# Kernel optimization log

Hardware: AMD Instinct MI355X
Metric: run time of the kernel (lower is better)

## Reference

```python
import jax, jax.numpy as jnp
import numpy as np

N = 100000
E = 1600000
IN_CH = 128
HID = 32
HEADS = 4
OUT_CH = 32
NEG_SLOPE = 0.2


def _gat_layer(x, W, a_src, a_dst, b, src, dst, heads, out_ch):
    """PyG-style GATConv (concat=True). x: [N, F_in]; returns [N, heads*out_ch]."""
    n = x.shape[0]
    h = (x @ W).reshape(n, heads, out_ch)                    # [N, H, C]
    alpha_s = jnp.einsum('nhc,hc->nh', h, a_src)             # [N, H]
    alpha_d = jnp.einsum('nhc,hc->nh', h, a_dst)             # [N, H]
    logits = jax.nn.leaky_relu(alpha_s[src] + alpha_d[dst], NEG_SLOPE)  # [E, H]
    # segment softmax over destination node
    m = jax.ops.segment_max(logits, dst, num_segments=n)
    m = jnp.where(jnp.isfinite(m), m, 0.0)
    p = jnp.exp(logits - m[dst])
    denom = jax.ops.segment_sum(p, dst, num_segments=n)
    alpha = p / (denom[dst] + 1e-16)                         # [E, H]
    msg = h[src] * alpha[..., None]                          # [E, H, C]
    out = jax.ops.segment_sum(msg, dst, num_segments=n)      # [N, H, C]
    return out.reshape(n, heads * out_ch) + b


def setup_inputs() -> dict:
    key = jax.random.key(0)
    ks = jax.random.split(key, 16)
    x = jax.random.normal(ks[0], (N, IN_CH), dtype=jnp.float32)
    edge_index = jax.random.randint(ks[1], (2, E), 0, N, dtype=jnp.int32)

    def glorot(k, shape):
        fan = shape[0] + shape[-1]
        return jax.random.normal(k, shape, dtype=jnp.float32) * np.sqrt(2.0 / fan)

    hid = HID * HEADS  # 128
    return {
        'x': x,
        'edge_index': edge_index,
        'W1': glorot(ks[2], (IN_CH, hid)),
        'a_src1': glorot(ks[3], (HEADS, HID)),
        'a_dst1': glorot(ks[4], (HEADS, HID)),
        'b1': jnp.zeros((hid,), jnp.float32),
        'W2': glorot(ks[5], (hid, hid)),
        'a_src2': glorot(ks[6], (HEADS, HID)),
        'a_dst2': glorot(ks[7], (HEADS, HID)),
        'b2': jnp.zeros((hid,), jnp.float32),
        'W3': glorot(ks[8], (hid, OUT_CH)),
        'a_src3': glorot(ks[9], (1, OUT_CH)),
        'a_dst3': glorot(ks[10], (1, OUT_CH)),
        'b3': jnp.zeros((OUT_CH,), jnp.float32),
    }


def reference(x, edge_index, W1, a_src1, a_dst1, b1, W2, a_src2, a_dst2, b2,
              W3, a_src3, a_dst3, b3):
    # add self-loops (PyG GATConv default add_self_loops=True)
    loop = jnp.arange(N, dtype=edge_index.dtype)
    src = jnp.concatenate([edge_index[0], loop])
    dst = jnp.concatenate([edge_index[1], loop])

    h = _gat_layer(x, W1, a_src1, a_dst1, b1, src, dst, HEADS, HID)
    h = jax.nn.elu(h)
    h = _gat_layer(h, W2, a_src2, a_dst2, b2, src, dst, HEADS, HID)
    h = jax.nn.elu(h)
    out = _gat_layer(h, W3, a_src3, a_dst3, b3, src, dst, 1, OUT_CH)
    return out
```

## Files before the change

### kernel.cpp

```cpp
#include <hip/hip_runtime.h>
#include <cstdint>

#define NN 100000
#define EE 1600000
#define ET (EE + NN)
#define NBUCK 782
#define BCAP 3584

typedef unsigned int u32;
typedef unsigned short u16;
typedef short bf16x8 __attribute__((ext_vector_type(8)));
typedef float f32x4 __attribute__((ext_vector_type(4)));

__device__ __forceinline__ u16 f2bf(float f) {
    union { float f; u32 i; } v; v.f = f;
    u32 r = v.i + 0x7FFFu + ((v.i >> 16) & 1u);
    return (u16)(r >> 16);
}
__device__ __forceinline__ float bf2f(u32 u) {
    union { u32 i; float f; } v; v.i = u << 16; return v.f;
}
__device__ __forceinline__ void get_edge(const int* __restrict__ ei, int e, int& s, int& d) {
    if (e < EE) { s = ei[e]; d = ei[EE + e]; }
    else { s = e - EE; d = s; }
}
__device__ __forceinline__ float leaky(float x) { return x > 0.f ? x : 0.2f * x; }

__global__ __launch_bounds__(256) void wprep_kernel(
    const float* __restrict__ W1, const float* __restrict__ W2, const float* __restrict__ W3,
    u16* __restrict__ wt1, u16* __restrict__ wt2, u16* __restrict__ wt3)
{
    int i = blockIdx.x * 256 + threadIdx.x;
    if (i < 16384)      { int c = i >> 7, k = i & 127; wt1[i] = f2bf(W1[k * 128 + c]); }
    else if (i < 32768) { int j = i - 16384; int c = j >> 7, k = j & 127; wt2[j] = f2bf(W2[k * 128 + c]); }
    else if (i < 36864) { int j = i - 32768; int c = j >> 7, k = j & 127; wt3[j] = f2bf(W3[k * 32 + c]); }
}

template<int OUTC, bool IN16>
__global__ __launch_bounds__(256) void gemm_mfma(
    const void* __restrict__ Xv, const u16* __restrict__ Wt16g,
    const float* __restrict__ asw, const float* __restrict__ adw,
    u16* __restrict__ Hout16, float* __restrict__ as_o, float* __restrict__ ad_o)
{
    constexpr int NT = OUTC / 16;
    constexpr int LDSU = (OUTC == 128) ? 13056 : 6528;
    constexpr int HS = (OUTC == 128) ? 132 : 36;
    __shared__ u32 lds[LDSU];
    u32* wl = lds + 64 * 68;

    const int tid = threadIdx.x;
    const int r0 = blockIdx.x * 64;

    if (IN16) {
        const u32* Xg = (const u32*)Xv;
        for (int i = tid; i < 64 * 64; i += 256) {
            int r = i >> 6, k2 = i & 63;
            u32 v = 0;
            if (r0 + r < NN) v = Xg[(size_t)(r0 + r) * 64 + k2];
            lds[r * 68 + k2] = v;
        }
    } else {
        const float* Xf = (const float*)Xv;
        for (int i = tid; i < 64 * 64; i += 256) {
            int r = i >> 6, k2 = i & 63;
            u32 v = 0;
            if (r0 + r < NN) {
                float2 f = *(const float2*)(Xf + (size_t)(r0 + r) * 128 + k2 * 2);
                v = (u32)f2bf(f.x) | ((u32)f2bf(f.y) << 16);
            }
            lds[r * 68 + k2] = v;
        }
    }
    {
        const u32* Wg = (const u32*)Wt16g;
        for (int i = tid; i < OUTC * 64; i += 256) {
            int c = i >> 6, k2 = i & 63;
            wl[c * 68 + k2] = Wg[i];
        }
    }
    __syncthreads();

    const int w = tid >> 6, l = tid & 63;
    const int lm = l & 15, q = l >> 4;

    f32x4 acc[NT];
    #pragma unroll
    for (int T = 0; T < NT; T++)
        #pragma unroll
        for (int r = 0; r < 4; r++) acc[T][r] = 0.f;

    #pragma unroll
    for (int kc = 0; kc < 4; kc++) {
        bf16x8 af = *(const bf16x8*)&lds[(16 * w + lm) * 68 + kc * 16 + q * 4];
        #pragma unroll
        for (int T = 0; T < NT; T++) {
            bf16x8 bfr = *(const bf16x8*)&wl[(16 * T + lm) * 68 + kc * 16 + q * 4];
            acc[T] = __builtin_amdgcn_mfma_f32_16x16x32_bf16(af, bfr, acc[T], 0, 0, 0);
        }
    }
    __syncthreads();

    float* hl = (float*)lds;
    #pragma unroll
    for (int T = 0; T < NT; T++)
        #pragma unroll
        for (int rg = 0; rg < 4; rg++)
            hl[(16 * w + q * 4 + rg) * HS + 16 * T + lm] = acc[T][rg];
    __syncthreads();

    for (int i = tid; i < 64 * (OUTC / 2); i += 256) {
        int r = i / (OUTC / 2), k2 = i % (OUTC / 2);
        int row = r0 + r;
        if (row < NN) {
            float a = hl[r * HS + k2 * 2];
            float b = hl[r * HS + k2 * 2 + 1];
            ((u32*)Hout16)[(size_t)row * (OUTC / 2) + k2] = (u32)f2bf(a) | ((u32)f2bf(b) << 16);
        }
    }
    if (OUTC == 128) {
        const int row = tid >> 2, part = tid & 3;
        const float* hp = &hl[row * HS + part * 32];
        const float* aw = asw + part * 32;
        const float* dw = adw + part * 32;
        float s = 0.f, d = 0.f;
        #pragma unroll
        for (int c = 0; c < 32; c++) { float hv = hp[c]; s += hv * aw[c]; d += hv * dw[c]; }
        const int grow = r0 + row;
        if (grow < NN) { as_o[(size_t)grow * 4 + part] = s; ad_o[(size_t)grow * 4 + part] = d; }
    } else {
        if (tid < 64) {
            const float* hp = &hl[tid * HS];
            float s = 0.f, d = 0.f;
            #pragma unroll
            for (int c = 0; c < 32; c++) { float hv = hp[c]; s += hv * asw[c]; d += hv * adw[c]; }
            const int grow = r0 + tid;
            if (grow < NN) { as_o[grow] = s; ad_o[grow] = d; }
        }
    }
}

__global__ __launch_bounds__(256) void bin_fill_kernel(const int* __restrict__ ei,
    int* __restrict__ gcur, u32* __restrict__ pairs)
{
    __shared__ int hist[NBUCK];
    __shared__ int base[NBUCK];
    const int t = threadIdx.x;
    for (int i = t; i < NBUCK; i += 256) hist[i] = 0;
    __syncthreads();
    const int chunk = (ET + gridDim.x - 1) / gridDim.x;
    const int e0 = blockIdx.x * chunk;
    const int e1 = min(e0 + chunk, ET);
    for (int e = e0 + t; e < e1; e += 256) {
        int s, d; get_edge(ei, e, s, d);
        atomicAdd(&hist[d >> 7], 1);
    }
    __syncthreads();
    for (int i = t; i < NBUCK; i += 256) {
        int c = hist[i];
        base[i] = c ? atomicAdd(&gcur[i], c) : 0;
        hist[i] = 0;
    }
    __syncthreads();
    for (int e = e0 + t; e < e1; e += 256) {
        int s, d; get_edge(ei, e, s, d);
        int b = d >> 7;
        int pos = atomicAdd(&hist[b], 1);
        pairs[(size_t)b * BCAP + base[b] + pos] = ((u32)(d & 127) << 25) | (u32)s;
    }
}

__global__ __launch_bounds__(1024) void bscan_kernel(const int* __restrict__ bcnt,
    int* __restrict__ bbase, int* __restrict__ rowp)
{
    __shared__ int lds[1024];
    const int t = threadIdx.x;
    int v = (t < NBUCK) ? bcnt[t] : 0;
    lds[t] = v;
    __syncthreads();
    for (int off = 1; off < 1024; off <<= 1) {
        int x = (t >= off) ? lds[t - off] : 0;
        __syncthreads();
        lds[t] += x;
        __syncthreads();
    }
    if (t < NBUCK) bbase[t] = lds[t] - v;
    if (t == 0) { bbase[NBUCK] = ET; rowp[NN] = ET; }
}

__global__ __launch_bounds__(256) void bucket_csr_kernel(const u32* __restrict__ pairs,
    const int* __restrict__ bcnt, const int* __restrict__ bbase,
    int* __restrict__ rowp, int* __restrict__ col)
{
    __shared__ int hist[128], scn[128];
    __shared__ int col_lds[BCAP];
    const int b = blockIdx.x;
    const int cbase = bbase[b];
    const int cnt = bcnt[b];
    const u32* pk0 = pairs + (size_t)b * BCAP;
    const int t = threadIdx.x;
    if (t < 128) hist[t] = 0;
    __syncthreads();
    for (int i = t; i < cnt; i += 256)
        atomicAdd(&hist[pk0[i] >> 25], 1);
    __syncthreads();
    if (t < 128) scn[t] = hist[t];
    __syncthreads();
    for (int off = 1; off < 128; off <<= 1) {
        int x = (t < 128 && t >= off) ? scn[t - off] : 0;
        __syncthreads();
        if (t < 128) scn[t] += x;
        __syncthreads();
    }
    if (t < 128) {
        int ex = scn[t] - hist[t];
        int node = b * 128 + t;
        if (node < NN) rowp[node] = cbase + ex;
        hist[t] = ex;
    }
    __syncthreads();
    for (int i = t; i < cnt; i += 256) {
        u32 pk = pk0[i];
        int pos = atomicAdd(&hist[pk >> 25], 1);
        if (pos < BCAP) col_lds[pos] = pk & 0x1FFFFFFu;
    }
    __syncthreads();
    for (int i = t; i < cnt; i += 256)
        col[cbase + i] = col_lds[i];
}

template<bool DOELU>
__global__ __launch_bounds__(256) void agg4_kernel(
    const int* __restrict__ rowp, const int* __restrict__ col,
    const float* __restrict__ as_, const float* __restrict__ ad_,
    const u16* __restrict__ Hb16, const float* __restrict__ bias,
    u16* __restrict__ outp16)
{
    const int lane = threadIdx.x & 63;
    const int node = blockIdx.x * 4 + (threadIdx.x >> 6);
    const int sub = lane & 15;
    const int h = lane >> 4;

    const int start = rowp[node];
    const int end   = rowp[node + 1];
    const float adv = ad_[(size_t)node * 4 + h];
    const char* hbase = (const char*)Hb16 + lane * 4;
    const float2 bv = *(const float2*)(bias + lane * 2);

    float m = -1e30f, den = 0.f, a0 = 0.f, a1 = 0.f;
    for (int j0 = start; j0 < end; j0 += 16) {
        const int j = j0 + sub;
        const bool valid = (j < end);
        const int s = valid ? col[j] : 0;
        const float lg = valid ? leaky(as_[(size_t)s * 4 + h] + adv) : -1e30f;
        float cm = lg;
        #pragma unroll
        for (int off = 8; off; off >>= 1) cm = fmaxf(cm, __shfl_xor(cm, off));
        const float mnew = fmaxf(m, cm);
        const float sc = __expf(m - mnew);
        a0 *= sc; a1 *= sc; den *= sc; m = mnew;
        const float p = valid ? __expf(lg - m) : 0.f;
        float ps = p;
        #pragma unroll
        for (int off = 8; off; off >>= 1) ps += __shfl_xor(ps, off);
        den += ps;
        const int soff = s << 8;
        int so[16]; float pi[16];
        #pragma unroll
        for (int i = 0; i < 16; i++) {
            so[i] = __shfl(soff, i);
            pi[i] = __shfl(p, (h << 4) | i);
        }
        #pragma unroll
        for (int i = 0; i < 16; i++) {
            u32 wv = *(const u32*)(hbase + so[i]);
            a0 += pi[i] * bf2f(wv & 0xffffu);
            a1 += pi[i] * bf2f(wv >> 16);
        }
    }
    const float rden = 1.f / (den + 1e-16f);
    float v0 = a0 * rden + bv.x;
    float v1 = a1 * rden + bv.y;
    if (DOELU) {
        v0 = v0 > 0.f ? v0 : (__expf(v0) - 1.f);
        v1 = v1 > 0.f ? v1 : (__expf(v1) - 1.f);
    }
    u32 pack = (u32)f2bf(v0) | ((u32)f2bf(v1) << 16);
    *(u32*)(outp16 + (size_t)node * 128 + lane * 2) = pack;
}

__global__ __launch_bounds__(256) void agg1_kernel(
    const int* __restrict__ rowp, const int* __restrict__ col,
    const float* __restrict__ as_, const float* __restrict__ ad_,
    const u16* __restrict__ Hb16, const float* __restrict__ bias,
    float* __restrict__ outp)
{
    const int t = threadIdx.x;
    const int lane = t & 31;
    const int node = blockIdx.x * 8 + (t >> 5);

    const int start = rowp[node];
    const int end   = rowp[node + 1];
    const float adv = ad_[node];
    const char* hbase = (const char*)Hb16 + lane * 2;
    const float bvv = bias[lane];

    float m = -1e30f, den = 0.f, acc = 0.f;
    for (int j0 = start; j0 < end; j0 += 32) {
        const int j = j0 + lane;
        const bool valid = (j < end);
        const int s = valid ? col[j] : 0;
        const float lg = valid ? leaky(as_[s] + adv) : -1e30f;
        float cm = lg;
        #pragma unroll
        for (int off = 16; off; off >>= 1) cm = fmaxf(cm, __shfl_xor(cm, off, 32));
        const float mnew = fmaxf(m, cm);
        const float sc = __expf(m - mnew);
        acc *= sc; den *= sc; m = mnew;
        const float p = valid ? __expf(lg - m) : 0.f;
        float ps = p;
        #pragma unroll
        for (int off = 16; off; off >>= 1) ps += __shfl_xor(ps, off, 32);
        den += ps;
        const int soff = s << 6;
        int so[32]; float pi[32];
        #pragma unroll
        for (int i = 0; i < 32; i++) {
            so[i] = __shfl(soff, i, 32);
            pi[i] = __shfl(p, i, 32);
        }
        #pragma unroll
        for (int i = 0; i < 32; i++)
            acc += pi[i] * bf2f((u32)*(const u16*)(hbase + so[i]));
    }
    outp[(size_t)node * 32 + lane] = acc / (den + 1e-16f) + bvv;
}

extern "C" void kernel_launch(void* const* d_in, const int* in_sizes, int n_in,
                              void* d_out, int out_size, void* d_ws, size_t ws_size,
                              hipStream_t stream)
{
    const float* x   = (const float*)d_in[0];
    const int*   ei  = (const int*)d_in[1];
    const float* W1  = (const float*)d_in[2];
    const float* as1 = (const float*)d_in[3];
    const float* ad1 = (const float*)d_in[4];
    const float* b1  = (const float*)d_in[5];
    const float* W2  = (const float*)d_in[6];
    const float* as2 = (const float*)d_in[7];
    const float* ad2 = (const float*)d_in[8];
    const float* b2  = (const float*)d_in[9];
    const float* W3  = (const float*)d_in[10];
    const float* as3 = (const float*)d_in[11];
    const float* ad3 = (const float*)d_in[12];
    const float* b3  = (const float*)d_in[13];
    float* outp = (float*)d_out;

    char* ws = (char*)d_ws;
    u16*   hb16  = (u16*)(ws);
    u16*   xb16  = (u16*)(ws + 25700000);
    u16*   h3b16 = (u16*)(ws + 51400000);
    float* asb   = (float*)(ws + 57900000);
    float* adb   = (float*)(ws + 59500000);
    int*   rowp  = (int*)(ws + 61100000);
    int*   col   = (int*)(ws + 61600000);
    u32*   pairs = (u32*)(ws + 68400032);
    int*   gcur  = (int*)(ws + 79700000);
    int*   bbase = (int*)(ws + 79704096);
    u16*   wt1   = (u16*)(ws + 79710000);
    u16*   wt2   = (u16*)(ws + 79750000);
    u16*   wt3   = (u16*)(ws + 79790000);

    const dim3 B(256);
    const int gG = (NN + 63) / 64;

    wprep_kernel<<<144, B, 0, stream>>>(W1, W2, W3, wt1, wt2, wt3);
    hipMemsetAsync(gcur, 0, NBUCK * 4, stream);
    bin_fill_kernel<<<256, B, 0, stream>>>(ei, gcur, pairs);
    bscan_kernel<<<1, dim3(1024), 0, stream>>>(gcur, bbase, rowp);
    bucket_csr_kernel<<<NBUCK, B, 0, stream>>>(pairs, gcur, bbase, rowp, col);

    gemm_mfma<128, false><<<gG, B, 0, stream>>>(x, wt1, as1, ad1, hb16, asb, adb);
    agg4_kernel<true><<<NN / 4, B, 0, stream>>>(rowp, col, asb, adb, hb16, b1, xb16);

    gemm_mfma<128, true><<<gG, B, 0, stream>>>(xb16, wt2, as2, ad2, hb16, asb, adb);
    agg4_kernel<true><<<NN / 4, B, 0, stream>>>(rowp, col, asb, adb, hb16, b2, xb16);

    gemm_mfma<32, true><<<gG, B, 0, stream>>>(xb16, wt3, as3, ad3, h3b16, asb, adb);
    agg1_kernel<<<NN / 8, B, 0, stream>>>(rowp, col, asb, adb, h3b16, b3, outp);
}
```

Measured before the change: 461.1 us.

## Fuse layer-1 GEMM, edge binning and weight prep; restructure aggregation per node-group

Merges the weight-prep, edge bin-fill and first-layer GEMM into one heterogeneous kernel launch, with the GEMM converting W1 from fp32 inline. This removes two launches and lets the independent GEMM and binning work run concurrently. The 4-head aggregation is rewritten so a 16-lane group handles a whole node with 16-byte gathers per edge and 8 channels per lane, passing probabilities through LDS instead of shuffles. The aim is more bytes per gather load and fewer shuffle instructions, at the cost of redundant per-head softmax math in every lane and extra LDS traffic.

```diff
diff --git a/kernel.cpp b/kernel.cpp
--- a/kernel.cpp
+++ b/kernel.cpp
@@ -6,6 +6,9 @@
 #define ET (EE + NN)
 #define NBUCK 782
 #define BCAP 3584
+#define G_GEMM 1563
+#define G_FILL 256
+#define G_WPREP 80
 
 typedef unsigned int u32;
 typedef unsigned short u16;
@@ -17,8 +20,11 @@
     u32 r = v.i + 0x7FFFu + ((v.i >> 16) & 1u);
     return (u16)(r >> 16);
 }
-__device__ __forceinline__ float bf2f(u32 u) {
+__device__ __forceinline__ float bf_lo(u32 u) {
     union { u32 i; float f; } v; v.i = u << 16; return v.f;
+}
+__device__ __forceinline__ float bf_hi(u32 u) {
+    union { u32 i; float f; } v; v.i = u & 0xffff0000u; return v.f;
 }
 __device__ __forceinline__ void get_edge(const int* __restrict__ ei, int e, int& s, int& d) {
     if (e < EE) { s = ei[e]; d = ei[EE + e]; }
@@ -26,30 +32,15 @@
 }
 __device__ __forceinline__ float leaky(float x) { return x > 0.f ? x : 0.2f * x; }
 
-__global__ __launch_bounds__(256) void wprep_kernel(
-    const float* __restrict__ W1, const float* __restrict__ W2, const float* __restrict__ W3,
-    u16* __restrict__ wt1, u16* __restrict__ wt2, u16* __restrict__ wt3)
-{
-    int i = blockIdx.x * 256 + threadIdx.x;
-    if (i < 16384)      { int c = i >> 7, k = i & 127; wt1[i] = f2bf(W1[k * 128 + c]); }
-    else if (i < 32768) { int j = i - 16384; int c = j >> 7, k = j & 127; wt2[j] = f2bf(W2[k * 128 + c]); }
-    else if (i < 36864) { int j = i - 32768; int c = j >> 7, k = j & 127; wt3[j] = f2bf(W3[k * 32 + c]); }
-}
-
-template<int OUTC, bool IN16>
-__global__ __launch_bounds__(256) void gemm_mfma(
-    const void* __restrict__ Xv, const u16* __restrict__ Wt16g,
+template<int OUTC, bool IN16, bool WCVT>
+__device__ __forceinline__ void gemm_body(int r0, u32* lds,
+    const void* __restrict__ Xv, const void* __restrict__ Wsrc,
     const float* __restrict__ asw, const float* __restrict__ adw,
-    u16* __restrict__ Hout16, float* __restrict__ as_o, float* __restrict__ ad_o)
+    u16* __restrict__ Hout16, float* __restrict__ as_o, float* __restrict__ ad_o, int tid)
 {
     constexpr int NT = OUTC / 16;
-    constexpr int LDSU = (OUTC == 128) ? 13056 : 6528;
     constexpr int HS = (OUTC == 128) ? 132 : 36;
-    __shared__ u32 lds[LDSU];
     u32* wl = lds + 64 * 68;
-
-    const int tid = threadIdx.x;
-    const int r0 = blockIdx.x * 64;
 
     if (IN16) {
         const u32* Xg = (const u32*)Xv;
@@ -71,8 +62,16 @@
             lds[r * 68 + k2] = v;
         }
     }
-    {
-        const u32* Wg = (const u32*)Wt16g;
+    if (WCVT) {
+        const float* Wf = (const float*)Wsrc;
+        for (int i = tid; i < 128 * 64; i += 256) {
+            int c = i & 127, k2 = i >> 7;
+            float f0 = Wf[(2 * k2) * 128 + c];
+            float f1 = Wf[(2 * k2 + 1) * 128 + c];
+            wl[c * 68 + k2] = (u32)f2bf(f0) | ((u32)f2bf(f1) << 16);
+        }
+    } else {
+        const u32* Wg = (const u32*)Wsrc;
         for (int i = tid; i < OUTC * 64; i += 256) {
             int c = i >> 6, k2 = i & 63;
             wl[c * 68 + k2] = Wg[i];
@@ -139,16 +138,13 @@
     }
 }
 
-__global__ __launch_bounds__(256) void bin_fill_kernel(const int* __restrict__ ei,
-    int* __restrict__ gcur, u32* __restrict__ pairs)
-{
-    __shared__ int hist[NBUCK];
-    __shared__ int base[NBUCK];
-    const int t = threadIdx.x;
+__device__ __forceinline__ void bin_fill_body(int bid, int* hist, int* base,
+    const int* __restrict__ ei, int* __restrict__ gcur, u32* __restrict__ pairs, int t)
+{
     for (int i = t; i < NBUCK; i += 256) hist[i] = 0;
     __syncthreads();
-    const int chunk = (ET + gridDim.x - 1) / gridDim.x;
-    const int e0 = blockIdx.x * chunk;
+    const int chunk = (ET + G_FILL - 1) / G_FILL;
+    const int e0 = bid * chunk;
     const int e1 = min(e0 + chunk, ET);
     for (int e = e0 + t; e < e1; e += 256) {
         int s, d; get_edge(ei, e, s, d);
@@ -167,6 +163,41 @@
         int pos = atomicAdd(&hist[b], 1);
         pairs[(size_t)b * BCAP + base[b] + pos] = ((u32)(d & 127) << 25) | (u32)s;
     }
+}
+
+__global__ __launch_bounds__(256) void fused1_kernel(
+    const float* __restrict__ X, const float* __restrict__ W1,
+    const float* __restrict__ as1, const float* __restrict__ ad1,
+    u16* __restrict__ hb16, float* __restrict__ asb, float* __restrict__ adb,
+    const int* __restrict__ ei, int* __restrict__ gcur, u32* __restrict__ pairs,
+    const float* __restrict__ W2, const float* __restrict__ W3,
+    u16* __restrict__ wt2, u16* __restrict__ wt3)
+{
+    __shared__ __align__(16) u32 smem[13056];
+    const int bid = blockIdx.x;
+    const int tid = threadIdx.x;
+    if (bid < G_GEMM) {
+        gemm_body<128, false, true>(bid * 64, smem, X, W1, as1, ad1, hb16, asb, adb, tid);
+    } else if (bid < G_GEMM + G_FILL) {
+        int* hist = (int*)smem;
+        bin_fill_body(bid - G_GEMM, hist, hist + NBUCK, ei, gcur, pairs, tid);
+    } else {
+        int i = (bid - G_GEMM - G_FILL) * 256 + tid;
+        if (i < 16384)      { int c = i >> 7, k = i & 127; wt2[i] = f2bf(W2[k * 128 + c]); }
+        else                { int j = i - 16384; int c = j >> 7, k = j & 127; wt3[j] = f2bf(W3[k * 32 + c]); }
+    }
+}
+
+template<int OUTC>
+__global__ __launch_bounds__(256) void gemm_mfma(
+    const void* __restrict__ Xv, const u16* __restrict__ Wt16g,
+    const float* __restrict__ asw, const float* __restrict__ adw,
+    u16* __restrict__ Hout16, float* __restrict__ as_o, float* __restrict__ ad_o)
+{
+    constexpr int LDSU = (OUTC == 128) ? 13056 : 6528;
+    __shared__ __align__(16) u32 lds[LDSU];
+    gemm_body<OUTC, true, false>(blockIdx.x * 64, lds, Xv, Wt16g, asw, adw,
+                                 Hout16, as_o, ad_o, threadIdx.x);
 }
 
 __global__ __launch_bounds__(1024) void bscan_kernel(const int* __restrict__ bcnt,
@@ -229,63 +260,109 @@
 }
 
 template<bool DOELU>
-__global__ __launch_bounds__(256) void agg4_kernel(
+__global__ __launch_bounds__(256) void agg4g_kernel(
     const int* __restrict__ rowp, const int* __restrict__ col,
     const float* __restrict__ as_, const float* __restrict__ ad_,
     const u16* __restrict__ Hb16, const float* __restrict__ bias,
     u16* __restrict__ outp16)
 {
-    const int lane = threadIdx.x & 63;
-    const int node = blockIdx.x * 4 + (threadIdx.x >> 6);
+    __shared__ float pex[4 * 288];
+    __shared__ u32   sex[4 * 64];
+    const int tid = threadIdx.x;
+    const int wv = tid >> 6;
+    const int lane = tid & 63;
+    const int g = lane >> 4;
     const int sub = lane & 15;
-    const int h = lane >> 4;
+    const int H = sub >> 2;
+    const int node = blockIdx.x * 16 + wv * 4 + g;
 
     const int start = rowp[node];
     const int end   = rowp[node + 1];
-    const float adv = ad_[(size_t)node * 4 + h];
-    const char* hbase = (const char*)Hb16 + lane * 4;
-    const float2 bv = *(const float2*)(bias + lane * 2);
-
-    float m = -1e30f, den = 0.f, a0 = 0.f, a1 = 0.f;
+    const float4 ad4 = ((const float4*)ad_)[node];
+    const float4* as4 = (const float4*)as_;
+    float* pb = &pex[wv * 288 + g * 68];
+    u32*   sb = &sex[wv * 64 + g * 16];
+    const char* hbase = (const char*)Hb16 + sub * 16;
+
+    float m0 = -1e30f, m1 = -1e30f, m2 = -1e30f, m3 = -1e30f;
+    float d0 = 0.f, d1 = 0.f, d2 = 0.f, d3 = 0.f;
+    float a[8];
+    #pragma unroll
+    for (int i = 0; i < 8; i++) a[i] = 0.f;
+
     for (int j0 = start; j0 < end; j0 += 16) {
         const int j = j0 + sub;
         const bool valid = (j < end);
         const int s = valid ? col[j] : 0;
-        const float lg = valid ? leaky(as_[(size_t)s * 4 + h] + adv) : -1e30f;
-        float cm = lg;
-        #pragma unroll
-        for (int off = 8; off; off >>= 1) cm = fmaxf(cm, __shfl_xor(cm, off));
-        const float mnew = fmaxf(m, cm);
-        const float sc = __expf(m - mnew);
-        a0 *= sc; a1 *= sc; den *= sc; m = mnew;
-        const float p = valid ? __expf(lg - m) : 0.f;
-        float ps = p;
-        #pragma unroll
-        for (int off = 8; off; off >>= 1) ps += __shfl_xor(ps, off);
-        den += ps;
-        const int soff = s << 8;
-        int so[16]; float pi[16];
+        const float4 av = as4[s];
+        float l0 = valid ? leaky(av.x + ad4.x) : -1e30f;
+        float l1 = valid ? leaky(av.y + ad4.y) : -1e30f;
+        float l2 = valid ? leaky(av.z + ad4.z) : -1e30f;
+        float l3 = valid ? leaky(av.w + ad4.w) : -1e30f;
+        float c0 = l0, c1 = l1, c2 = l2, c3 = l3;
+        #pragma unroll
+        for (int off = 8; off; off >>= 1) {
+            c0 = fmaxf(c0, __shfl_xor(c0, off, 16));
+            c1 = fmaxf(c1, __shfl_xor(c1, off, 16));
+            c2 = fmaxf(c2, __shfl_xor(c2, off, 16));
+            c3 = fmaxf(c3, __shfl_xor(c3, off, 16));
+        }
+        const float n0 = fmaxf(m0, c0), n1 = fmaxf(m1, c1);
+        const float n2 = fmaxf(m2, c2), n3 = fmaxf(m3, c3);
+        const float s0 = __expf(m0 - n0), s1 = __expf(m1 - n1);
+        const float s2 = __expf(m2 - n2), s3 = __expf(m3 - n3);
+        float p0 = valid ? __expf(l0 - n0) : 0.f;
+        float p1 = valid ? __expf(l1 - n1) : 0.f;
+        float p2 = valid ? __expf(l2 - n2) : 0.f;
+        float p3 = valid ? __expf(l3 - n3) : 0.f;
+        float q0 = p0, q1 = p1, q2 = p2, q3 = p3;
+        #pragma unroll
+        for (int off = 8; off; off >>= 1) {
+            q0 += __shfl_xor(q0, off, 16);
+            q1 += __shfl_xor(q1, off, 16);
+            q2 += __shfl_xor(q2, off, 16);
+            q3 += __shfl_xor(q3, off, 16);
+        }
+        d0 = d0 * s0 + q0; d1 = d1 * s1 + q1;
+        d2 = d2 * s2 + q2; d3 = d3 * s3 + q3;
+        m0 = n0; m1 = n1; m2 = n2; m3 = n3;
+        const float scH = (H == 0) ? s0 : (H == 1) ? s1 : (H == 2) ? s2 : s3;
+        #pragma unroll
+        for (int i = 0; i < 8; i++) a[i] *= scH;
+        pb[sub * 4 + 0] = p0; pb[sub * 4 + 1] = p1;
+        pb[sub * 4 + 2] = p2; pb[sub * 4 + 3] = p3;
+        sb[sub] = (u32)s << 8;
+        u32 so[16]; float pi[16];
+        #pragma unroll
+        for (int i = 0; i < 16; i++) { so[i] = sb[i]; pi[i] = pb[i * 4 + H]; }
         #pragma unroll
         for (int i = 0; i < 16; i++) {
-            so[i] = __shfl(soff, i);
-            pi[i] = __shfl(p, (h << 4) | i);
-        }
-        #pragma unroll
-        for (int i = 0; i < 16; i++) {
-            u32 wv = *(const u32*)(hbase + so[i]);
-            a0 += pi[i] * bf2f(wv & 0xffffu);
-            a1 += pi[i] * bf2f(wv >> 16);
-        }
-    }
-    const float rden = 1.f / (den + 1e-16f);
-    float v0 = a0 * rden + bv.x;
-    float v1 = a1 * rden + bv.y;
+            const uint4 w = *(const uint4*)(hbase + so[i]);
+            a[0] += pi[i] * bf_lo(w.x); a[1] += pi[i] * bf_hi(w.x);
+            a[2] += pi[i] * bf_lo(w.y); a[3] += pi[i] * bf_hi(w.y);
+            a[4] += pi[i] * bf_lo(w.z); a[5] += pi[i] * bf_hi(w.z);
+            a[6] += pi[i] * bf_lo(w.w); a[7] += pi[i] * bf_hi(w.w);
+        }
+    }
+    const float denH = (H == 0) ? d0 : (H == 1) ? d1 : (H == 2) ? d2 : d3;
+    const float r = 1.f / (denH + 1e-16f);
+    const float4 b0 = ((const float4*)bias)[sub * 2];
+    const float4 b1 = ((const float4*)bias)[sub * 2 + 1];
+    float v[8];
+    v[0] = a[0] * r + b0.x; v[1] = a[1] * r + b0.y;
+    v[2] = a[2] * r + b0.z; v[3] = a[3] * r + b0.w;
+    v[4] = a[4] * r + b1.x; v[5] = a[5] * r + b1.y;
+    v[6] = a[6] * r + b1.z; v[7] = a[7] * r + b1.w;
     if (DOELU) {
-        v0 = v0 > 0.f ? v0 : (__expf(v0) - 1.f);
-        v1 = v1 > 0.f ? v1 : (__expf(v1) - 1.f);
-    }
-    u32 pack = (u32)f2bf(v0) | ((u32)f2bf(v1) << 16);
-    *(u32*)(outp16 + (size_t)node * 128 + lane * 2) = pack;
+        #pragma unroll
+        for (int i = 0; i < 8; i++) v[i] = v[i] > 0.f ? v[i] : (__expf(v[i]) - 1.f);
+    }
+    uint4 o;
+    o.x = (u32)f2bf(v[0]) | ((u32)f2bf(v[1]) << 16);
+    o.y = (u32)f2bf(v[2]) | ((u32)f2bf(v[3]) << 16);
+    o.z = (u32)f2bf(v[4]) | ((u32)f2bf(v[5]) << 16);
+    o.w = (u32)f2bf(v[6]) | ((u32)f2bf(v[7]) << 16);
+    *(uint4*)(outp16 + (size_t)node * 128 + sub * 8) = o;
 }
 
 __global__ __launch_bounds__(256) void agg1_kernel(
@@ -330,7 +407,7 @@
         }
         #pragma unroll
         for (int i = 0; i < 32; i++)
-            acc += pi[i] * bf2f((u32)*(const u16*)(hbase + so[i]));
+            acc += pi[i] * bf_lo((u32)*(const u16*)(hbase + so[i]));
     }
     outp[(size_t)node * 32 + lane] = acc / (den + 1e-16f) + bvv;
 }
@@ -366,25 +443,23 @@
     u32*   pairs = (u32*)(ws + 68400032);
     int*   gcur  = (int*)(ws + 79700000);
     int*   bbase = (int*)(ws + 79704096);
-    u16*   wt1   = (u16*)(ws + 79710000);
     u16*   wt2   = (u16*)(ws + 79750000);
     u16*   wt3   = (u16*)(ws + 79790000);
 
     const dim3 B(256);
     const int gG = (NN + 63) / 64;
 
-    wprep_kernel<<<144, B, 0, stream>>>(W1, W2, W3, wt1, wt2, wt3);
     hipMemsetAsync(gcur, 0, NBUCK * 4, stream);
-    bin_fill_kernel<<<256, B, 0, stream>>>(ei, gcur, pairs);
+    fused1_kernel<<<G_GEMM + G_FILL + G_WPREP, B, 0, stream>>>(
+        x, W1, as1, ad1, hb16, asb, adb, ei, gcur, pairs, W2, W3, wt2, wt3);
     bscan_kernel<<<1, dim3(1024), 0, stream>>>(gcur, bbase, rowp);
     bucket_csr_kernel<<<NBUCK, B, 0, stream>>>(pairs, gcur, bbase, rowp, col);
 
-    gemm_mfma<128, false><<<gG, B, 0, stream>>>(x, wt1, as1, ad1, hb16, asb, adb);
-    agg4_kernel<true><<<NN / 4, B, 0, stream>>>(rowp, col, asb, adb, hb16, b1, xb16);
-
-    gemm_mfma<128, true><<<gG, B, 0, stream>>>(xb16, wt2, as2, ad2, hb16, asb, adb);
-    agg4_kernel<true><<<NN / 4, B, 0, stream>>>(rowp, col, asb, adb, hb16, b2, xb16);
-
-    gemm_mfma<32, true><<<gG, B, 0, stream>>>(xb16, wt3, as3, ad3, h3b16, asb, adb);
+    agg4g_kernel<true><<<NN / 16, B, 0, stream>>>(rowp, col, asb, adb, hb16, b1, xb16);
+
+    gemm_mfma<128><<<gG, B, 0, stream>>>(xb16, wt2, as2, ad2, hb16, asb, adb);
+    agg4g_kernel<true><<<NN / 16, B, 0, stream>>>(rowp, col, asb, adb, hb16, b2, xb16);
+
+    gemm_mfma<32><<<gG, B, 0, stream>>>(xb16, wt3, as3, ad3, h3b16, asb, adb);
     agg1_kernel<<<NN / 8, B, 0, stream>>>(rowp, col, asb, adb, h3b16, b3, outp);
 }
```

Result: slower. 475.6 us (+3.2%).
